# Optimization experiments

Hardware: AMD Instinct MI355X
Metric: run time of the kernel (lower is better)

The kernel has to match this reference:

```python
import jax, jax.numpy as jnp
import numpy as np

NUM_HEADS = 8
QUERY_HEAD_DIM = 32
POS_HEAD_DIM = 4
EMBED_DIM = 512
POS_DIM = 192
SEQ_LEN = 1024
BATCH = 8
IN_PROJ_DIM = (QUERY_HEAD_DIM * 2 + POS_HEAD_DIM) * NUM_HEADS  # 544


def setup_inputs() -> dict:
    key = jax.random.key(0)
    k1, k2, k3, k4, k5 = jax.random.split(key, 5)
    x = jax.random.normal(k1, (SEQ_LEN, BATCH, EMBED_DIM), dtype=jnp.float32)
    pos_emb = jax.random.normal(k2, (1, 2 * SEQ_LEN - 1, POS_DIM), dtype=jnp.float32)
    key_padding_mask = jnp.zeros((BATCH, SEQ_LEN), dtype=bool)
    # in_proj: ScaledLinear(embed_dim -> in_proj_dim) with initial_scale qhd**-0.25
    scale_in = QUERY_HEAD_DIM ** (-0.25) / np.sqrt(EMBED_DIM)
    W_in = jax.random.normal(k3, (EMBED_DIM, IN_PROJ_DIM), dtype=jnp.float32) * scale_in
    b_in = jax.random.normal(k4, (IN_PROJ_DIM,), dtype=jnp.float32) * 0.01
    # linear_pos: ScaledLinear(pos_dim -> num_heads*pos_head_dim), no bias, scale 0.05
    W_pos = jax.random.normal(k5, (POS_DIM, NUM_HEADS * POS_HEAD_DIM), dtype=jnp.float32) * (0.05 / np.sqrt(POS_DIM))
    return {"x": x, "pos_emb": pos_emb, "W_in": W_in, "b_in": b_in,
            "W_pos": W_pos, "key_padding_mask": key_padding_mask}


def reference(x, pos_emb, W_in, b_in, W_pos, key_padding_mask):
    S, B, _ = x.shape
    H, QH, PH = NUM_HEADS, QUERY_HEAD_DIM, POS_HEAD_DIM
    qd = H * QH
    xp = x @ W_in + b_in                          # (S, B, in_proj_dim)
    q = xp[..., :qd].reshape(S, B, H, QH)
    k = xp[..., qd:2 * qd].reshape(S, B, H, QH)   # Whiten/Balancer are identity in eval
    p = xp[..., 2 * qd:].reshape(S, B, H, PH)
    # content scores: (H, B, T, Sk)
    attn_scores = jnp.einsum('tbhd,sbhd->hbts', q, k)
    # positional scores
    pe = (pos_emb @ W_pos).reshape(2 * S - 1, H, PH)          # (2S-1, H, PH)
    pos_scores = jnp.einsum('tbhd,nhd->hbtn', p, pe)          # (H, B, T, 2S-1)
    # relative shift: out[h,b,t,j] = pos_scores[h,b,t, (S-1) - t + j]
    idx = (S - 1) - jnp.arange(S)[:, None] + jnp.arange(S)[None, :]  # (S, S)
    shifted = jnp.take_along_axis(pos_scores, idx[None, None, :, :], axis=-1)
    attn_scores = attn_scores + shifted
    # key padding mask: True positions get -1000 (as in masked_fill)
    attn_scores = jnp.where(key_padding_mask[None, :, None, :], -1000.0, attn_scores)
    return jax.nn.softmax(attn_scores, axis=-1)  # (H, B, T, S)
```

## Files before the change

### kernel.cpp

```cpp
#include <hip/hip_runtime.h>

#define SEQ  1024
#define BATCH 8
#define NH   8
#define EMB  512
#define QHD  32
#define PHD  4
#define PDIM 192
#define NPROJ 544
#define NPE  2047

typedef float nf4 __attribute__((ext_vector_type(4)));
typedef short bf16x8 __attribute__((ext_vector_type(8)));
typedef float f32x4 __attribute__((ext_vector_type(4)));

__device__ __forceinline__ unsigned short f2bf_rne(float f) {
    unsigned int u = __float_as_uint(f);
    unsigned int r = (u + 0x7fffu + ((u >> 16) & 1u)) >> 16;
    return (unsigned short)r;
}
__device__ __forceinline__ float bf2f(unsigned short b) {
    return __uint_as_float(((unsigned int)b) << 16);
}

__global__ __launch_bounds__(256) void convx_kernel(const float* __restrict__ x,
                                                    unsigned short* __restrict__ xhi,
                                                    unsigned short* __restrict__ xlo) {
    int i = (blockIdx.x * 256 + threadIdx.x) * 8;
    float4 a = *(const float4*)(x + i);
    float4 b = *(const float4*)(x + i + 4);
    ushort4 h0, l0, h1, l1;
    h0.x = f2bf_rne(a.x); l0.x = f2bf_rne(a.x - bf2f(h0.x));
    h0.y = f2bf_rne(a.y); l0.y = f2bf_rne(a.y - bf2f(h0.y));
    h0.z = f2bf_rne(a.z); l0.z = f2bf_rne(a.z - bf2f(h0.z));
    h0.w = f2bf_rne(a.w); l0.w = f2bf_rne(a.w - bf2f(h0.w));
    h1.x = f2bf_rne(b.x); l1.x = f2bf_rne(b.x - bf2f(h1.x));
    h1.y = f2bf_rne(b.y); l1.y = f2bf_rne(b.y - bf2f(h1.y));
    h1.z = f2bf_rne(b.z); l1.z = f2bf_rne(b.z - bf2f(h1.z));
    h1.w = f2bf_rne(b.w); l1.w = f2bf_rne(b.w - bf2f(h1.w));
    *(ushort4*)(xhi + i) = h0; *(ushort4*)(xhi + i + 4) = h1;
    *(ushort4*)(xlo + i) = l0; *(ushort4*)(xlo + i + 4) = l1;
}

__global__ __launch_bounds__(256) void convw_kernel(const float* __restrict__ W,
                                                    unsigned short* __restrict__ whT,
                                                    unsigned short* __restrict__ wlT) {
    __shared__ float tile[32][33];
    const int n0 = blockIdx.x * 32, k0 = blockIdx.y * 32;
    const int c = threadIdx.x & 31, r0 = threadIdx.x >> 5;
#pragma unroll
    for (int i = 0; i < 4; ++i) {
        int r = r0 + i * 8;
        tile[r][c] = W[(size_t)(k0 + r) * NPROJ + n0 + c];
    }
    __syncthreads();
#pragma unroll
    for (int i = 0; i < 4; ++i) {
        int n = r0 + i * 8;
        float v = tile[c][n];
        unsigned short h = f2bf_rne(v);
        unsigned short l = f2bf_rne(v - bf2f(h));
        whT[(size_t)(n0 + n) * 512 + k0 + c] = h;
        wlT[(size_t)(n0 + n) * 512 + k0 + c] = l;
    }
}

__global__ __launch_bounds__(128) void pe_kernel(const float* __restrict__ pos_emb,
                                                 const float* __restrict__ W_pos,
                                                 unsigned short* __restrict__ peg) {
    const int n = blockIdx.x * 128 + threadIdx.x;
    const int h = blockIdx.y;
    if (n >= NPE) return;
    const float* pr = pos_emb + (size_t)n * PDIM;
    float a0 = 0.f, a1 = 0.f, a2 = 0.f, a3 = 0.f;
    for (int c = 0; c < PDIM; c += 4) {
        float4 pv = *(const float4*)(pr + c);
#pragma unroll
        for (int cc = 0; cc < 4; ++cc) {
            float pvc = cc == 0 ? pv.x : cc == 1 ? pv.y : cc == 2 ? pv.z : pv.w;
            float4 w4 = *(const float4*)(W_pos + (c + cc) * 32 + h * 4);
            a0 += pvc * w4.x; a1 += pvc * w4.y; a2 += pvc * w4.z; a3 += pvc * w4.w;
        }
    }
    ushort4 o;
    o.x = f2bf_rne(a0); o.y = f2bf_rne(a1); o.z = f2bf_rne(a2); o.w = f2bf_rne(a3);
    *(ushort4*)(peg + ((size_t)h * NPE + n) * 4) = o;
}

__global__ __launch_bounds__(256) void inproj_kernel(const unsigned short* __restrict__ xhi,
                                                     const unsigned short* __restrict__ xlo,
                                                     const unsigned short* __restrict__ whT,
                                                     const unsigned short* __restrict__ wlT,
                                                     const float* __restrict__ bias,
                                                     unsigned short* __restrict__ qhi,
                                                     unsigned short* __restrict__ qlo,
                                                     unsigned short* __restrict__ khi,
                                                     unsigned short* __restrict__ klo,
                                                     float* __restrict__ pws) {
    __shared__ __align__(16) unsigned short xh_l[8][128][8];
    __shared__ __align__(16) unsigned short xl_l[8][128][8];
    __shared__ __align__(16) unsigned short wh_l[8][32][8];
    __shared__ __align__(16) unsigned short wl_l[8][32][8];

    const int tid = threadIdx.x, lane = tid & 63, w = tid >> 6;
    const int la = lane & 15, lb = lane >> 4;
    const int m0 = blockIdx.x * 128, n0 = blockIdx.y * 32;

    const int mx = tid >> 1, k8x = (tid & 1) * 4;
    const int nw = tid >> 3, k8w = tid & 7;

    f32x4 acc[2][2];
#pragma unroll
    for (int mt = 0; mt < 2; ++mt)
#pragma unroll
        for (int nt = 0; nt < 2; ++nt) acc[mt][nt] = (f32x4){0.f, 0.f, 0.f, 0.f};

    for (int step = 0; step < 8; ++step) {
        const int k0 = step * 64;
        const unsigned short* sxh = xhi + (size_t)(m0 + mx) * 512 + k0 + k8x * 8;
        const unsigned short* sxl = xlo + (size_t)(m0 + mx) * 512 + k0 + k8x * 8;
#pragma unroll
        for (int j = 0; j < 4; ++j) {
            *(uint4*)&xh_l[k8x + j][mx][0] = *(const uint4*)(sxh + j * 8);
            *(uint4*)&xl_l[k8x + j][mx][0] = *(const uint4*)(sxl + j * 8);
        }
        *(uint4*)&wh_l[k8w][nw][0] = *(const uint4*)(whT + (size_t)(n0 + nw) * 512 + k0 + k8w * 8);
        *(uint4*)&wl_l[k8w][nw][0] = *(const uint4*)(wlT + (size_t)(n0 + nw) * 512 + k0 + k8w * 8);
        __syncthreads();
#pragma unroll
        for (int ks = 0; ks < 2; ++ks) {
            bf16x8 bh[2], bl[2], ah[2], al[2];
#pragma unroll
            for (int mt = 0; mt < 2; ++mt) {
                bh[mt] = *(const bf16x8*)&xh_l[ks * 4 + lb][w * 32 + mt * 16 + la][0];
                bl[mt] = *(const bf16x8*)&xl_l[ks * 4 + lb][w * 32 + mt * 16 + la][0];
            }
#pragma unroll
            for (int nt = 0; nt < 2; ++nt) {
                ah[nt] = *(const bf16x8*)&wh_l[ks * 4 + lb][nt * 16 + la][0];
                al[nt] = *(const bf16x8*)&wl_l[ks * 4 + lb][nt * 16 + la][0];
            }
#pragma unroll
            for (int mt = 0; mt < 2; ++mt)
#pragma unroll
                for (int nt = 0; nt < 2; ++nt) {
                    acc[mt][nt] = __builtin_amdgcn_mfma_f32_16x16x32_bf16(ah[nt], bh[mt], acc[mt][nt], 0, 0, 0);
                    acc[mt][nt] = __builtin_amdgcn_mfma_f32_16x16x32_bf16(ah[nt], bl[mt], acc[mt][nt], 0, 0, 0);
                    acc[mt][nt] = __builtin_amdgcn_mfma_f32_16x16x32_bf16(al[nt], bh[mt], acc[mt][nt], 0, 0, 0);
                }
        }
        __syncthreads();
    }

    const int by = blockIdx.y;
#pragma unroll
    for (int mt = 0; mt < 2; ++mt) {
        const int m = m0 + w * 32 + mt * 16 + la;
        const int s = m >> 3, bb = m & 7;
#pragma unroll
        for (int nt = 0; nt < 2; ++nt) {
            const int dloc = nt * 16 + lb * 4;
            float4 b4 = *(const float4*)(bias + n0 + dloc);
            float v0 = acc[mt][nt][0] + b4.x;
            float v1 = acc[mt][nt][1] + b4.y;
            float v2 = acc[mt][nt][2] + b4.z;
            float v3 = acc[mt][nt][3] + b4.w;
            if (by < 16) {
                const int h = by & 7;
                size_t base = (((size_t)(h * 8 + bb) * SEQ + s) * 32 + dloc);
                ushort4 hi, lo;
                hi.x = f2bf_rne(v0); lo.x = f2bf_rne(v0 - bf2f(hi.x));
                hi.y = f2bf_rne(v1); lo.y = f2bf_rne(v1 - bf2f(hi.y));
                hi.z = f2bf_rne(v2); lo.z = f2bf_rne(v2 - bf2f(hi.z));
                hi.w = f2bf_rne(v3); lo.w = f2bf_rne(v3 - bf2f(hi.w));
                if (by < 8) {
                    *(ushort4*)(qhi + base) = hi;
                    *(ushort4*)(qlo + base) = lo;
                } else {
                    *(ushort4*)(khi + base) = hi;
                    *(ushort4*)(klo + base) = lo;
                }
            } else {
                const int h = nt * 4 + lb;
                float4 o; o.x = v0; o.y = v1; o.z = v2; o.w = v3;
                *(float4*)(pws + ((size_t)(h * 8 + bb) * SEQ + s) * 4) = o;
            }
        }
    }
}

__global__ __launch_bounds__(256, 3) void attn_kernel(const unsigned short* __restrict__ qhi,
                                                      const unsigned short* __restrict__ qlo,
                                                      const unsigned short* __restrict__ khi,
                                                      const unsigned short* __restrict__ klo,
                                                      const float* __restrict__ pws,
                                                      const unsigned short* __restrict__ peg,
                                                      const unsigned char* __restrict__ km,
                                                      float* __restrict__ out) {
    __shared__ unsigned long long pe_lds[1040];
    __shared__ float red_m[16][4];
    __shared__ float red_s[16][4];

    const int bid = blockIdx.x;
    const int hb = bid & 63;
    const int h = hb >> 3, b = hb & 7;
    const int t0 = (bid >> 6) * 16;
    const int tid = threadIdx.x, lane = tid & 63;
    const int j_s = tid >> 6;
    const int la = lane & 15, lb = lane >> 4;

    const int nbase = (SEQ - 1) - t0 - 15;
    const unsigned long long* pegq = (const unsigned long long*)peg + (size_t)h * NPE + nbase;
#pragma unroll
    for (int it = 0; it < 5; ++it) {
        int idx = it * 256 + tid;
        if (idx < 1039) pe_lds[idx] = pegq[idx];
    }
    __syncthreads();

    const int t = t0 + la;
    const size_t qoff = ((size_t)hb * SEQ + t) * 32 + lb * 8;
    const bf16x8 bqh = *(const bf16x8*)(qhi + qoff);
    const bf16x8 bql = *(const bf16x8*)(qlo + qoff);

    const unsigned short* khb = khi + (size_t)hb * (SEQ * 32);
    const unsigned short* klb = klo + (size_t)hb * (SEQ * 32);

    f32x4 acc[16];
#pragma unroll
    for (int m = 0; m < 16; ++m) acc[m] = (f32x4){0.f, 0.f, 0.f, 0.f};

#pragma unroll
    for (int m = 0; m < 16; ++m) {
        const int srow = j_s * 256 + m * 16 + la;
        const bf16x8 ah = *(const bf16x8*)(khb + (size_t)srow * 32 + lb * 8);
        const bf16x8 al = *(const bf16x8*)(klb + (size_t)srow * 32 + lb * 8);
        acc[m] = __builtin_amdgcn_mfma_f32_16x16x32_bf16(ah, bqh, acc[m], 0, 0, 0);
        acc[m] = __builtin_amdgcn_mfma_f32_16x16x32_bf16(ah, bql, acc[m], 0, 0, 0);
        acc[m] = __builtin_amdgcn_mfma_f32_16x16x32_bf16(al, bqh, acc[m], 0, 0, 0);
    }

    const float4 pvv = *(const float4*)(pws + ((size_t)hb * SEQ + t) * 4);
    const int lane_off = j_s * 256 + lb * 4 + 15 - la;
#pragma unroll
    for (int m = 0; m < 16; ++m) {
        const int o = lane_off + m * 16;
#pragma unroll
        for (int j = 0; j < 4; ++j) {
            unsigned long long v = pe_lds[o + j];
            unsigned int w0 = (unsigned int)v, w1 = (unsigned int)(v >> 32);
            float e0 = __uint_as_float(w0 << 16);
            float e1 = __uint_as_float(w0 & 0xffff0000u);
            float e2 = __uint_as_float(w1 << 16);
            float e3 = __uint_as_float(w1 & 0xffff0000u);
            acc[m][j] += pvv.x * e0 + pvv.y * e1 + pvv.z * e2 + pvv.w * e3;
        }
    }

    const unsigned int* kmw = (const unsigned int*)(km + b * SEQ);
#pragma unroll
    for (int m = 0; m < 16; ++m) {
        unsigned int mk = kmw[j_s * 64 + m * 4 + lb];
        if (mk & 0x000000ffu) acc[m][0] = -1000.f;
        if (mk & 0x0000ff00u) acc[m][1] = -1000.f;
        if (mk & 0x00ff0000u) acc[m][2] = -1000.f;
        if (mk & 0xff000000u) acc[m][3] = -1000.f;
    }

    float mx = -3.4e38f;
#pragma unroll
    for (int m = 0; m < 16; ++m)
        mx = fmaxf(mx, fmaxf(fmaxf(acc[m][0], acc[m][1]), fmaxf(acc[m][2], acc[m][3])));
    mx = fmaxf(mx, __shfl_xor(mx, 16, 64));
    mx = fmaxf(mx, __shfl_xor(mx, 32, 64));
    if (lane < 16) red_m[lane][j_s] = mx;
    __syncthreads();
    const float fm = fmaxf(fmaxf(red_m[la][0], red_m[la][1]),
                           fmaxf(red_m[la][2], red_m[la][3]));
    float sum = 0.f;
#pragma unroll
    for (int m = 0; m < 16; ++m) {
        acc[m][0] = __expf(acc[m][0] - fm);
        acc[m][1] = __expf(acc[m][1] - fm);
        acc[m][2] = __expf(acc[m][2] - fm);
        acc[m][3] = __expf(acc[m][3] - fm);
        sum += (acc[m][0] + acc[m][1]) + (acc[m][2] + acc[m][3]);
    }
    sum += __shfl_xor(sum, 16, 64);
    sum += __shfl_xor(sum, 32, 64);
    if (lane < 16) red_s[lane][j_s] = sum;
    __syncthreads();
    const float inv = 1.0f / ((red_s[la][0] + red_s[la][1]) + (red_s[la][2] + red_s[la][3]));

    float* op = out + ((size_t)hb * SEQ + t) * SEQ;
#pragma unroll
    for (int m = 0; m < 16; ++m) {
        nf4 o;
        o.x = acc[m][0] * inv;
        o.y = acc[m][1] * inv;
        o.z = acc[m][2] * inv;
        o.w = acc[m][3] * inv;
        __builtin_nontemporal_store(o, (nf4*)(op + j_s * 256 + m * 16 + lb * 4));
    }
}

extern "C" void kernel_launch(void* const* d_in, const int* in_sizes, int n_in,
                              void* d_out, int out_size, void* d_ws, size_t ws_size,
                              hipStream_t stream) {
    const float* x       = (const float*)d_in[0];
    const float* pos_emb = (const float*)d_in[1];
    const float* W_in    = (const float*)d_in[2];
    const float* b_in    = (const float*)d_in[3];
    const float* W_pos   = (const float*)d_in[4];
    const unsigned char* km = (const unsigned char*)d_in[5];
    float* out = (float*)d_out;

    char* ws = (char*)d_ws;
    const size_t MB = 1024 * 1024;
    unsigned short* qhi = (unsigned short*)(ws);
    unsigned short* qlo = (unsigned short*)(ws + 4 * MB);
    unsigned short* khi = (unsigned short*)(ws + 8 * MB);
    unsigned short* klo = (unsigned short*)(ws + 12 * MB);
    float*          pws = (float*)(ws + 16 * MB);
    unsigned short* peg = (unsigned short*)(ws + 17 * MB);
    unsigned short* xhi = (unsigned short*)(ws + 18 * MB);
    unsigned short* xlo = (unsigned short*)(ws + 26 * MB);
    unsigned short* whT = (unsigned short*)(ws + 34 * MB);
    unsigned short* wlT = (unsigned short*)(ws + 35 * MB);

    hipLaunchKernelGGL(convx_kernel, dim3(2048), dim3(256), 0, stream, x, xhi, xlo);
    hipLaunchKernelGGL(convw_kernel, dim3(17, 16), dim3(256), 0, stream, W_in, whT, wlT);
    hipLaunchKernelGGL(pe_kernel, dim3(16, 8), dim3(128), 0, stream, pos_emb, W_pos, peg);
    hipLaunchKernelGGL(inproj_kernel, dim3(64, 17), dim3(256), 0, stream,
                       xhi, xlo, whT, wlT, b_in, qhi, qlo, khi, klo, pws);
    hipLaunchKernelGGL(attn_kernel, dim3(4096), dim3(256), 0, stream,
                       qhi, qlo, khi, klo, pws, peg, km, out);
}
```

Measured before the change: 160.3 us.

## Fuse x bf16 split into inproj and process 32 query rows per attention block

Removes the standalone convx kernel: the in-projection kernel now reads fp32 x and splits it into bf16 hi/lo pairs while staging into LDS, which saves a write and reread of the split copies. The attention kernel now handles 32 query rows per block instead of 16. Each loaded K fragment and the positional-embedding LDS tile are reused for two query tiles, and the grid is halved. Occupancy drops from 3 to 2 blocks per CU because of the doubled accumulator register use.

```diff
diff --git a/kernel.cpp b/kernel.cpp
--- a/kernel.cpp
+++ b/kernel.cpp
@@ -9,6 +9,7 @@
 #define PDIM 192
 #define NPROJ 544
 #define NPE  2047
+#define TBLK 32
 
 typedef float nf4 __attribute__((ext_vector_type(4)));
 typedef short bf16x8 __attribute__((ext_vector_type(8)));
@@ -22,24 +23,17 @@
 __device__ __forceinline__ float bf2f(unsigned short b) {
     return __uint_as_float(((unsigned int)b) << 16);
 }
-
-__global__ __launch_bounds__(256) void convx_kernel(const float* __restrict__ x,
-                                                    unsigned short* __restrict__ xhi,
-                                                    unsigned short* __restrict__ xlo) {
-    int i = (blockIdx.x * 256 + threadIdx.x) * 8;
-    float4 a = *(const float4*)(x + i);
-    float4 b = *(const float4*)(x + i + 4);
-    ushort4 h0, l0, h1, l1;
-    h0.x = f2bf_rne(a.x); l0.x = f2bf_rne(a.x - bf2f(h0.x));
-    h0.y = f2bf_rne(a.y); l0.y = f2bf_rne(a.y - bf2f(h0.y));
-    h0.z = f2bf_rne(a.z); l0.z = f2bf_rne(a.z - bf2f(h0.z));
-    h0.w = f2bf_rne(a.w); l0.w = f2bf_rne(a.w - bf2f(h0.w));
-    h1.x = f2bf_rne(b.x); l1.x = f2bf_rne(b.x - bf2f(h1.x));
-    h1.y = f2bf_rne(b.y); l1.y = f2bf_rne(b.y - bf2f(h1.y));
-    h1.z = f2bf_rne(b.z); l1.z = f2bf_rne(b.z - bf2f(h1.z));
-    h1.w = f2bf_rne(b.w); l1.w = f2bf_rne(b.w - bf2f(h1.w));
-    *(ushort4*)(xhi + i) = h0; *(ushort4*)(xhi + i + 4) = h1;
-    *(ushort4*)(xlo + i) = l0; *(ushort4*)(xlo + i + 4) = l1;
+__device__ __forceinline__ void cvt8(const float4 a, const float4 b, uint4& hi, uint4& lo) {
+    unsigned short h0 = f2bf_rne(a.x), h1 = f2bf_rne(a.y), h2 = f2bf_rne(a.z), h3 = f2bf_rne(a.w);
+    unsigned short h4 = f2bf_rne(b.x), h5 = f2bf_rne(b.y), h6 = f2bf_rne(b.z), h7 = f2bf_rne(b.w);
+    unsigned short l0 = f2bf_rne(a.x - bf2f(h0)), l1 = f2bf_rne(a.y - bf2f(h1));
+    unsigned short l2 = f2bf_rne(a.z - bf2f(h2)), l3 = f2bf_rne(a.w - bf2f(h3));
+    unsigned short l4 = f2bf_rne(b.x - bf2f(h4)), l5 = f2bf_rne(b.y - bf2f(h5));
+    unsigned short l6 = f2bf_rne(b.z - bf2f(h6)), l7 = f2bf_rne(b.w - bf2f(h7));
+    hi.x = (unsigned)h0 | ((unsigned)h1 << 16); hi.y = (unsigned)h2 | ((unsigned)h3 << 16);
+    hi.z = (unsigned)h4 | ((unsigned)h5 << 16); hi.w = (unsigned)h6 | ((unsigned)h7 << 16);
+    lo.x = (unsigned)l0 | ((unsigned)l1 << 16); lo.y = (unsigned)l2 | ((unsigned)l3 << 16);
+    lo.z = (unsigned)l4 | ((unsigned)l5 << 16); lo.w = (unsigned)l6 | ((unsigned)l7 << 16);
 }
 
 __global__ __launch_bounds__(256) void convw_kernel(const float* __restrict__ W,
@@ -87,8 +81,7 @@
     *(ushort4*)(peg + ((size_t)h * NPE + n) * 4) = o;
 }
 
-__global__ __launch_bounds__(256) void inproj_kernel(const unsigned short* __restrict__ xhi,
-                                                     const unsigned short* __restrict__ xlo,
+__global__ __launch_bounds__(256) void inproj_kernel(const float* __restrict__ x,
                                                      const unsigned short* __restrict__ whT,
                                                      const unsigned short* __restrict__ wlT,
                                                      const float* __restrict__ bias,
@@ -117,12 +110,15 @@
 
     for (int step = 0; step < 8; ++step) {
         const int k0 = step * 64;
-        const unsigned short* sxh = xhi + (size_t)(m0 + mx) * 512 + k0 + k8x * 8;
-        const unsigned short* sxl = xlo + (size_t)(m0 + mx) * 512 + k0 + k8x * 8;
+        const float* sx = x + (size_t)(m0 + mx) * EMB + k0 + k8x * 8;
 #pragma unroll
         for (int j = 0; j < 4; ++j) {
-            *(uint4*)&xh_l[k8x + j][mx][0] = *(const uint4*)(sxh + j * 8);
-            *(uint4*)&xl_l[k8x + j][mx][0] = *(const uint4*)(sxl + j * 8);
+            float4 a = *(const float4*)(sx + j * 8);
+            float4 b = *(const float4*)(sx + j * 8 + 4);
+            uint4 hi, lo;
+            cvt8(a, b, hi, lo);
+            *(uint4*)&xh_l[k8x + j][mx][0] = hi;
+            *(uint4*)&xl_l[k8x + j][mx][0] = lo;
         }
         *(uint4*)&wh_l[k8w][nw][0] = *(const uint4*)(whT + (size_t)(n0 + nw) * 512 + k0 + k8w * 8);
         *(uint4*)&wl_l[k8w][nw][0] = *(const uint4*)(wlT + (size_t)(n0 + nw) * 512 + k0 + k8w * 8);
@@ -189,7 +185,7 @@
     }
 }
 
-__global__ __launch_bounds__(256, 3) void attn_kernel(const unsigned short* __restrict__ qhi,
+__global__ __launch_bounds__(256, 2) void attn_kernel(const unsigned short* __restrict__ qhi,
                                                       const unsigned short* __restrict__ qlo,
                                                       const unsigned short* __restrict__ khi,
                                                       const unsigned short* __restrict__ klo,
@@ -197,63 +193,81 @@
                                                       const unsigned short* __restrict__ peg,
                                                       const unsigned char* __restrict__ km,
                                                       float* __restrict__ out) {
-    __shared__ unsigned long long pe_lds[1040];
-    __shared__ float red_m[16][4];
-    __shared__ float red_s[16][4];
+    __shared__ unsigned long long pe_lds[1056];
+    __shared__ float red_m[2][16][4];
+    __shared__ float red_s[2][16][4];
 
     const int bid = blockIdx.x;
     const int hb = bid & 63;
     const int h = hb >> 3, b = hb & 7;
-    const int t0 = (bid >> 6) * 16;
+    const int t0 = (bid >> 6) * TBLK;
     const int tid = threadIdx.x, lane = tid & 63;
     const int j_s = tid >> 6;
     const int la = lane & 15, lb = lane >> 4;
 
-    const int nbase = (SEQ - 1) - t0 - 15;
+    const int nbase = (SEQ - 1) - t0 - (TBLK - 1);
     const unsigned long long* pegq = (const unsigned long long*)peg + (size_t)h * NPE + nbase;
 #pragma unroll
     for (int it = 0; it < 5; ++it) {
         int idx = it * 256 + tid;
-        if (idx < 1039) pe_lds[idx] = pegq[idx];
+        if (idx < 1055) pe_lds[idx] = pegq[idx];
     }
     __syncthreads();
 
-    const int t = t0 + la;
-    const size_t qoff = ((size_t)hb * SEQ + t) * 32 + lb * 8;
-    const bf16x8 bqh = *(const bf16x8*)(qhi + qoff);
-    const bf16x8 bql = *(const bf16x8*)(qlo + qoff);
+    const int t_a = t0 + la, t_b = t0 + 16 + la;
+    const size_t qoffa = ((size_t)hb * SEQ + t_a) * 32 + lb * 8;
+    const size_t qoffb = ((size_t)hb * SEQ + t_b) * 32 + lb * 8;
+    const bf16x8 bqh0 = *(const bf16x8*)(qhi + qoffa);
+    const bf16x8 bql0 = *(const bf16x8*)(qlo + qoffa);
+    const bf16x8 bqh1 = *(const bf16x8*)(qhi + qoffb);
+    const bf16x8 bql1 = *(const bf16x8*)(qlo + qoffb);
 
     const unsigned short* khb = khi + (size_t)hb * (SEQ * 32);
     const unsigned short* klb = klo + (size_t)hb * (SEQ * 32);
 
-    f32x4 acc[16];
-#pragma unroll
-    for (int m = 0; m < 16; ++m) acc[m] = (f32x4){0.f, 0.f, 0.f, 0.f};
+    f32x4 acc0[16], acc1[16];
+#pragma unroll
+    for (int m = 0; m < 16; ++m) { acc0[m] = (f32x4){0.f,0.f,0.f,0.f}; acc1[m] = (f32x4){0.f,0.f,0.f,0.f}; }
 
 #pragma unroll
     for (int m = 0; m < 16; ++m) {
         const int srow = j_s * 256 + m * 16 + la;
         const bf16x8 ah = *(const bf16x8*)(khb + (size_t)srow * 32 + lb * 8);
         const bf16x8 al = *(const bf16x8*)(klb + (size_t)srow * 32 + lb * 8);
-        acc[m] = __builtin_amdgcn_mfma_f32_16x16x32_bf16(ah, bqh, acc[m], 0, 0, 0);
-        acc[m] = __builtin_amdgcn_mfma_f32_16x16x32_bf16(ah, bql, acc[m], 0, 0, 0);
-        acc[m] = __builtin_amdgcn_mfma_f32_16x16x32_bf16(al, bqh, acc[m], 0, 0, 0);
-    }
-
-    const float4 pvv = *(const float4*)(pws + ((size_t)hb * SEQ + t) * 4);
-    const int lane_off = j_s * 256 + lb * 4 + 15 - la;
-#pragma unroll
-    for (int m = 0; m < 16; ++m) {
-        const int o = lane_off + m * 16;
+        acc0[m] = __builtin_amdgcn_mfma_f32_16x16x32_bf16(ah, bqh0, acc0[m], 0, 0, 0);
+        acc1[m] = __builtin_amdgcn_mfma_f32_16x16x32_bf16(ah, bqh1, acc1[m], 0, 0, 0);
+        acc0[m] = __builtin_amdgcn_mfma_f32_16x16x32_bf16(ah, bql0, acc0[m], 0, 0, 0);
+        acc1[m] = __builtin_amdgcn_mfma_f32_16x16x32_bf16(ah, bql1, acc1[m], 0, 0, 0);
+        acc0[m] = __builtin_amdgcn_mfma_f32_16x16x32_bf16(al, bqh0, acc0[m], 0, 0, 0);
+        acc1[m] = __builtin_amdgcn_mfma_f32_16x16x32_bf16(al, bqh1, acc1[m], 0, 0, 0);
+    }
+
+    const float4 pv0 = *(const float4*)(pws + ((size_t)hb * SEQ + t_a) * 4);
+    const float4 pv1 = *(const float4*)(pws + ((size_t)hb * SEQ + t_b) * 4);
+    const int off0 = j_s * 256 + lb * 4 + (TBLK - 1) - la;
+    const int off1 = off0 - 16;
+#pragma unroll
+    for (int m = 0; m < 16; ++m) {
 #pragma unroll
         for (int j = 0; j < 4; ++j) {
-            unsigned long long v = pe_lds[o + j];
-            unsigned int w0 = (unsigned int)v, w1 = (unsigned int)(v >> 32);
-            float e0 = __uint_as_float(w0 << 16);
-            float e1 = __uint_as_float(w0 & 0xffff0000u);
-            float e2 = __uint_as_float(w1 << 16);
-            float e3 = __uint_as_float(w1 & 0xffff0000u);
-            acc[m][j] += pvv.x * e0 + pvv.y * e1 + pvv.z * e2 + pvv.w * e3;
+            {
+                unsigned long long v = pe_lds[off0 + m * 16 + j];
+                unsigned int w0 = (unsigned int)v, w1 = (unsigned int)(v >> 32);
+                float e0 = __uint_as_float(w0 << 16);
+                float e1 = __uint_as_float(w0 & 0xffff0000u);
+                float e2 = __uint_as_float(w1 << 16);
+                float e3 = __uint_as_float(w1 & 0xffff0000u);
+                acc0[m][j] += pv0.x * e0 + pv0.y * e1 + pv0.z * e2 + pv0.w * e3;
+            }
+            {
+                unsigned long long v = pe_lds[off1 + m * 16 + j];
+                unsigned int w0 = (unsigned int)v, w1 = (unsigned int)(v >> 32);
+                float e0 = __uint_as_float(w0 << 16);
+                float e1 = __uint_as_float(w0 & 0xffff0000u);
+                float e2 = __uint_as_float(w1 << 16);
+                float e3 = __uint_as_float(w1 & 0xffff0000u);
+                acc1[m][j] += pv1.x * e0 + pv1.y * e1 + pv1.z * e2 + pv1.w * e3;
+            }
         }
     }
 
@@ -261,46 +275,54 @@
 #pragma unroll
     for (int m = 0; m < 16; ++m) {
         unsigned int mk = kmw[j_s * 64 + m * 4 + lb];
-        if (mk & 0x000000ffu) acc[m][0] = -1000.f;
-        if (mk & 0x0000ff00u) acc[m][1] = -1000.f;
-        if (mk & 0x00ff0000u) acc[m][2] = -1000.f;
-        if (mk & 0xff000000u) acc[m][3] = -1000.f;
-    }
-
-    float mx = -3.4e38f;
-#pragma unroll
-    for (int m = 0; m < 16; ++m)
-        mx = fmaxf(mx, fmaxf(fmaxf(acc[m][0], acc[m][1]), fmaxf(acc[m][2], acc[m][3])));
-    mx = fmaxf(mx, __shfl_xor(mx, 16, 64));
-    mx = fmaxf(mx, __shfl_xor(mx, 32, 64));
-    if (lane < 16) red_m[lane][j_s] = mx;
+        if (mk & 0x000000ffu) { acc0[m][0] = -1000.f; acc1[m][0] = -1000.f; }
+        if (mk & 0x0000ff00u) { acc0[m][1] = -1000.f; acc1[m][1] = -1000.f; }
+        if (mk & 0x00ff0000u) { acc0[m][2] = -1000.f; acc1[m][2] = -1000.f; }
+        if (mk & 0xff000000u) { acc0[m][3] = -1000.f; acc1[m][3] = -1000.f; }
+    }
+
+    float mx0 = -3.4e38f, mx1 = -3.4e38f;
+#pragma unroll
+    for (int m = 0; m < 16; ++m) {
+        mx0 = fmaxf(mx0, fmaxf(fmaxf(acc0[m][0], acc0[m][1]), fmaxf(acc0[m][2], acc0[m][3])));
+        mx1 = fmaxf(mx1, fmaxf(fmaxf(acc1[m][0], acc1[m][1]), fmaxf(acc1[m][2], acc1[m][3])));
+    }
+    mx0 = fmaxf(mx0, __shfl_xor(mx0, 16, 64)); mx0 = fmaxf(mx0, __shfl_xor(mx0, 32, 64));
+    mx1 = fmaxf(mx1, __shfl_xor(mx1, 16, 64)); mx1 = fmaxf(mx1, __shfl_xor(mx1, 32, 64));
+    if (lane < 16) { red_m[0][lane][j_s] = mx0; red_m[1][lane][j_s] = mx1; }
     __syncthreads();
-    const float fm = fmaxf(fmaxf(red_m[la][0], red_m[la][1]),
-                           fmaxf(red_m[la][2], red_m[la][3]));
-    float sum = 0.f;
-#pragma unroll
-    for (int m = 0; m < 16; ++m) {
-        acc[m][0] = __expf(acc[m][0] - fm);
-        acc[m][1] = __expf(acc[m][1] - fm);
-        acc[m][2] = __expf(acc[m][2] - fm);
-        acc[m][3] = __expf(acc[m][3] - fm);
-        sum += (acc[m][0] + acc[m][1]) + (acc[m][2] + acc[m][3]);
-    }
-    sum += __shfl_xor(sum, 16, 64);
-    sum += __shfl_xor(sum, 32, 64);
-    if (lane < 16) red_s[lane][j_s] = sum;
+    const float fm0 = fmaxf(fmaxf(red_m[0][la][0], red_m[0][la][1]),
+                            fmaxf(red_m[0][la][2], red_m[0][la][3]));
+    const float fm1 = fmaxf(fmaxf(red_m[1][la][0], red_m[1][la][1]),
+                            fmaxf(red_m[1][la][2], red_m[1][la][3]));
+    float s0 = 0.f, s1 = 0.f;
+#pragma unroll
+    for (int m = 0; m < 16; ++m) {
+        acc0[m][0] = __expf(acc0[m][0] - fm0); acc0[m][1] = __expf(acc0[m][1] - fm0);
+        acc0[m][2] = __expf(acc0[m][2] - fm0); acc0[m][3] = __expf(acc0[m][3] - fm0);
+        s0 += (acc0[m][0] + acc0[m][1]) + (acc0[m][2] + acc0[m][3]);
+        acc1[m][0] = __expf(acc1[m][0] - fm1); acc1[m][1] = __expf(acc1[m][1] - fm1);
+        acc1[m][2] = __expf(acc1[m][2] - fm1); acc1[m][3] = __expf(acc1[m][3] - fm1);
+        s1 += (acc1[m][0] + acc1[m][1]) + (acc1[m][2] + acc1[m][3]);
+    }
+    s0 += __shfl_xor(s0, 16, 64); s0 += __shfl_xor(s0, 32, 64);
+    s1 += __shfl_xor(s1, 16, 64); s1 += __shfl_xor(s1, 32, 64);
+    if (lane < 16) { red_s[0][lane][j_s] = s0; red_s[1][lane][j_s] = s1; }
     __syncthreads();
-    const float inv = 1.0f / ((red_s[la][0] + red_s[la][1]) + (red_s[la][2] + red_s[la][3]));
-
-    float* op = out + ((size_t)hb * SEQ + t) * SEQ;
-#pragma unroll
-    for (int m = 0; m < 16; ++m) {
-        nf4 o;
-        o.x = acc[m][0] * inv;
-        o.y = acc[m][1] * inv;
-        o.z = acc[m][2] * inv;
-        o.w = acc[m][3] * inv;
-        __builtin_nontemporal_store(o, (nf4*)(op + j_s * 256 + m * 16 + lb * 4));
+    const float inv0 = 1.0f / ((red_s[0][la][0] + red_s[0][la][1]) + (red_s[0][la][2] + red_s[0][la][3]));
+    const float inv1 = 1.0f / ((red_s[1][la][0] + red_s[1][la][1]) + (red_s[1][la][2] + red_s[1][la][3]));
+
+    float* op0 = out + ((size_t)hb * SEQ + t_a) * SEQ + j_s * 256;
+    float* op1 = out + ((size_t)hb * SEQ + t_b) * SEQ + j_s * 256;
+#pragma unroll
+    for (int m = 0; m < 16; ++m) {
+        nf4 o0, o1;
+        o0.x = acc0[m][0] * inv0; o0.y = acc0[m][1] * inv0;
+        o0.z = acc0[m][2] * inv0; o0.w = acc0[m][3] * inv0;
+        o1.x = acc1[m][0] * inv1; o1.y = acc1[m][1] * inv1;
+        o1.z = acc1[m][2] * inv1; o1.w = acc1[m][3] * inv1;
+        __builtin_nontemporal_store(o0, (nf4*)(op0 + m * 16 + lb * 4));
+        __builtin_nontemporal_store(o1, (nf4*)(op1 + m * 16 + lb * 4));
     }
 }
 
@@ -323,16 +345,13 @@
     unsigned short* klo = (unsigned short*)(ws + 12 * MB);
     float*          pws = (float*)(ws + 16 * MB);
     unsigned short* peg = (unsigned short*)(ws + 17 * MB);
-    unsigned short* xhi = (unsigned short*)(ws + 18 * MB);
-    unsigned short* xlo = (unsigned short*)(ws + 26 * MB);
-    unsigned short* whT = (unsigned short*)(ws + 34 * MB);
-    unsigned short* wlT = (unsigned short*)(ws + 35 * MB);
-
-    hipLaunchKernelGGL(convx_kernel, dim3(2048), dim3(256), 0, stream, x, xhi, xlo);
+    unsigned short* whT = (unsigned short*)(ws + 18 * MB);
+    unsigned short* wlT = (unsigned short*)(ws + 19 * MB);
+
     hipLaunchKernelGGL(convw_kernel, dim3(17, 16), dim3(256), 0, stream, W_in, whT, wlT);
     hipLaunchKernelGGL(pe_kernel, dim3(16, 8), dim3(128), 0, stream, pos_emb, W_pos, peg);
     hipLaunchKernelGGL(inproj_kernel, dim3(64, 17), dim3(256), 0, stream,
-                       xhi, xlo, whT, wlT, b_in, qhi, qlo, khi, klo, pws);
-    hipLaunchKernelGGL(attn_kernel, dim3(4096), dim3(256), 0, stream,
+                       x, whT, wlT, b_in, qhi, qlo, khi, klo, pws);
+    hipLaunchKernelGGL(attn_kernel, dim3(2048), dim3(256), 0, stream,
                        qhi, qlo, khi, klo, pws, peg, km, out);
 }
```

Result: slower. 169.4 us (+5.7%).
